# Optimization experiments

Measured on AMD Instinct MI355X. Metric: run time of the kernel, lower is better.

The kernel has to match this reference:

```python
import jax, jax.numpy as jnp
import numpy as np

T, B, IN = 64, 4096, 145
H1, H2 = 150, 32


def _lstm_layer(x, w_ih, w_hh, b_ih, b_hh):
    """Single LSTM layer, PyTorch gate order (i, f, g, o).
    x: (T, B, in_dim); w_ih: (4H, in_dim); w_hh: (4H, H); biases: (4H,).
    Returns hidden sequence (T, B, H)."""
    H = w_hh.shape[1]
    Bsz = x.shape[1]
    # Precompute input contribution for all timesteps at once (one big GEMM).
    xg = jnp.einsum('tbi,gi->tbg', x, w_ih) + (b_ih + b_hh)  # (T, B, 4H)
    w_hh_t = w_hh.T  # (H, 4H)

    def step(carry, xg_t):
        h, c = carry
        gates = xg_t + h @ w_hh_t  # (B, 4H)
        i, f, g, o = jnp.split(gates, 4, axis=-1)
        i = jax.nn.sigmoid(i)
        f = jax.nn.sigmoid(f)
        g = jnp.tanh(g)
        o = jax.nn.sigmoid(o)
        c = f * c + i * g
        h = o * jnp.tanh(c)
        return (h, c), h

    h0 = jnp.zeros((Bsz, H), x.dtype)
    c0 = jnp.zeros((Bsz, H), x.dtype)
    _, hs = jax.lax.scan(step, (h0, c0), xg)
    return hs  # (T, B, H)


def _init_lstm_params(key, in_dim, hidden):
    # PyTorch init: U(-k, k) with k = 1/sqrt(hidden)
    k = 1.0 / np.sqrt(hidden)
    ks = jax.random.split(key, 4)
    w_ih = jax.random.uniform(ks[0], (4 * hidden, in_dim), jnp.float32, -k, k)
    w_hh = jax.random.uniform(ks[1], (4 * hidden, hidden), jnp.float32, -k, k)
    b_ih = jax.random.uniform(ks[2], (4 * hidden,), jnp.float32, -k, k)
    b_hh = jax.random.uniform(ks[3], (4 * hidden,), jnp.float32, -k, k)
    return w_ih, w_hh, b_ih, b_hh


def setup_inputs() -> dict:
    key = jax.random.key(0)
    kx, k0, k1, k2 = jax.random.split(key, 4)
    x = jax.random.normal(kx, (T, B, IN), jnp.float32)
    w_ih_l0, w_hh_l0, b_ih_l0, b_hh_l0 = _init_lstm_params(k0, IN, H1)
    w_ih_l1, w_hh_l1, b_ih_l1, b_hh_l1 = _init_lstm_params(k1, H1, H1)
    w_ih_l2, w_hh_l2, b_ih_l2, b_hh_l2 = _init_lstm_params(k2, H1, H2)
    return {
        'x': x,
        'w_ih_l0': w_ih_l0, 'w_hh_l0': w_hh_l0, 'b_ih_l0': b_ih_l0, 'b_hh_l0': b_hh_l0,
        'w_ih_l1': w_ih_l1, 'w_hh_l1': w_hh_l1, 'b_ih_l1': b_ih_l1, 'b_hh_l1': b_hh_l1,
        'w_ih_l2': w_ih_l2, 'w_hh_l2': w_hh_l2, 'b_ih_l2': b_ih_l2, 'b_hh_l2': b_hh_l2,
    }


def reference(x,
              w_ih_l0, w_hh_l0, b_ih_l0, b_hh_l0,
              w_ih_l1, w_hh_l1, b_ih_l1, b_hh_l1,
              w_ih_l2, w_hh_l2, b_ih_l2, b_hh_l2):
    # temporal_model1: 2-layer LSTM (145 -> 150 -> 150)
    h = _lstm_layer(x, w_ih_l0, w_hh_l0, b_ih_l0, b_hh_l0)
    h = _lstm_layer(h, w_ih_l1, w_hh_l1, b_ih_l1, b_hh_l1)
    # temporal_model2: 1-layer LSTM (150 -> 32)
    out2 = _lstm_layer(h, w_ih_l2, w_hh_l2, b_ih_l2, b_hh_l2)
    return out2  # (T, B, 32)
```

## Files before the change

### kernel.cpp

```cpp
#include <hip/hip_runtime.h>


typedef _Float16 f16;
typedef _Float16 f16x8 __attribute__((ext_vector_type(8)));
typedef _Float16 f16x4 __attribute__((ext_vector_type(4)));
typedef float f32x4 __attribute__((ext_vector_type(4)));

#define T_STEPS 64
#define BATCH 4096

__device__ __forceinline__ float fexp(float x) {
  return __builtin_amdgcn_exp2f(x * 1.44269504088896340736f);
}
__device__ __forceinline__ float sigf(float x) {
  return __builtin_amdgcn_rcpf(1.0f + fexp(-x));
}
__device__ __forceinline__ float tanh_f(float x) {
  return 1.0f - 2.0f * __builtin_amdgcn_rcpf(1.0f + fexp(2.0f * x));
}

#define BAR_LGKM() asm volatile("s_waitcnt lgkmcnt(0)\n\ts_barrier" ::: "memory")

__global__ __launch_bounds__(256) void prep_w(
    const float* __restrict__ wih0, const float* __restrict__ bih0, const float* __restrict__ bhh0,
    const float* __restrict__ wih1, const float* __restrict__ bih1, const float* __restrict__ bhh1,
    f16* __restrict__ wprep0, f16* __restrict__ wprep1,
    float* __restrict__ bias0, float* __restrict__ bias1) {
  int idx = blockIdx.x * 256 + threadIdx.x;
  constexpr int WE = 640 * 168;
  if (idx < WE) {
    int c = idx / 168, k = idx - c * 168;
    int gate = c / 160, cg = c - gate * 160;
    float v = (cg < 150 && k < 145) ? wih0[(size_t)(gate * 150 + cg) * 145 + k] : 0.f;
    wprep0[idx] = (f16)v;
  } else if (idx < 2 * WE) {
    int e = idx - WE;
    int c = e / 168, k = e - c * 168;
    int gate = c / 160, cg = c - gate * 160;
    float v = (cg < 150 && k < 150) ? wih1[(size_t)(gate * 150 + cg) * 150 + k] : 0.f;
    wprep1[e] = (f16)v;
  } else if (idx < 2 * WE + 640) {
    int c = idx - 2 * WE;
    int gate = c / 160, cg = c - gate * 160;
    bias0[c] = (cg < 150) ? (bih0[gate * 150 + cg] + bhh0[gate * 150 + cg]) : 0.f;
  } else if (idx < 2 * WE + 1280) {
    int c = idx - 2 * WE - 640;
    int gate = c / 160, cg = c - gate * 160;
    bias1[c] = (cg < 150) ? (bih1[gate * 150 + cg] + bhh1[gate * 150 + cg]) : 0.f;
  }
}

template <int IN_DIM, int SRC_F16>
__global__ __launch_bounds__(512, 2) void gemm_xg3(
    const float* __restrict__ xin_f32, const f16* __restrict__ xin_f16,
    const f16* __restrict__ wprep, const float* __restrict__ bias_pre,
    f16* __restrict__ xg) {
  constexpr int ASTR = 168;
  __shared__ __align__(16) f16 A_lds[128 * ASTR];
  __shared__ __align__(16) float bias_lds[640];
  const int tid = threadIdx.x;
  const int mtile = blockIdx.x;
  const int g0 = mtile * 128;

  if constexpr (SRC_F16) {
#pragma unroll
    for (int q = 0; q < 6; ++q) {
      int i = q * 512 + tid;
      if (i < 2688)
        *(f16x8*)(&A_lds[i * 8]) = *(const f16x8*)(xin_f16 + (size_t)g0 * ASTR + (size_t)i * 8);
    }
  } else {
#pragma unroll
    for (int q = 0; q < 10; ++q) {
      int idx = q * 512 + tid;
      int r = idx / 40, c4 = (idx - r * 40) * 4;
      f16x4 o;
      if (c4 + 4 <= IN_DIM) {
        f32x4 v;
        __builtin_memcpy(&v, xin_f32 + (size_t)(g0 + r) * IN_DIM + c4, 16);
#pragma unroll
        for (int j = 0; j < 4; ++j) o[j] = (f16)v[j];
      } else {
#pragma unroll
        for (int j = 0; j < 4; ++j)
          o[j] = (c4 + j < IN_DIM) ? (f16)xin_f32[(size_t)(g0 + r) * IN_DIM + c4 + j] : (f16)0.f;
      }
      *(f16x4*)(&A_lds[r * ASTR + c4]) = o;
    }
  }
  if (tid < 160) *(f32x4*)(&bias_lds[tid * 4]) = *(const f32x4*)(bias_pre + tid * 4);
  __syncthreads();

  const int l = tid & 63, wv = tid >> 6;
  const int p = wv >> 1, cq = wv & 1;
  const int lrow = l & 15, lk8 = (l >> 4) * 8, r0 = (l >> 4) * 4;
  const int arow0 = (2 * p) * 16 + lrow;
  const size_t rg0 = (size_t)(mtile * 8 + 2 * p);

  const f16* wb = wprep + (size_t)(cq * 32 + lrow) * ASTR + lk8;

  f16x8 b0[5], b1[5], n0[5], n1[5];
#pragma unroll
  for (int kc = 0; kc < 5; ++kc) {
    b0[kc] = *(const f16x8*)(wb + kc * 32);
    b1[kc] = *(const f16x8*)(wb + 16 * ASTR + kc * 32);
  }

  for (int ch = 0; ch < 10; ++ch) {
    if (ch < 9) {
      const f16* wn = wb + (size_t)(ch + 1) * 64 * ASTR;
#pragma unroll
      for (int kc = 0; kc < 5; ++kc) {
        n0[kc] = *(const f16x8*)(wn + kc * 32);
        n1[kc] = *(const f16x8*)(wn + 16 * ASTR + kc * 32);
      }
    }
    const int c0 = ch * 64 + cq * 32 + lrow;
    const float bs0 = bias_lds[c0], bs1 = bias_lds[c0 + 16];
    f32x4 a00 = {bs0, bs0, bs0, bs0}, a01 = {bs1, bs1, bs1, bs1};
    f32x4 a10 = a00, a11 = a01;
#pragma unroll
    for (int kc = 0; kc < 5; ++kc) {
      f16x8 a0 = *(const f16x8*)(&A_lds[arow0 * ASTR + kc * 32 + lk8]);
      f16x8 a1 = *(const f16x8*)(&A_lds[(arow0 + 16) * ASTR + kc * 32 + lk8]);
      a00 = __builtin_amdgcn_mfma_f32_16x16x32_f16(a0, b0[kc], a00, 0, 0, 0);
      a01 = __builtin_amdgcn_mfma_f32_16x16x32_f16(a0, b1[kc], a01, 0, 0, 0);
      a10 = __builtin_amdgcn_mfma_f32_16x16x32_f16(a1, b0[kc], a10, 0, 0, 0);
      a11 = __builtin_amdgcn_mfma_f32_16x16x32_f16(a1, b1[kc], a11, 0, 0, 0);
    }
    {
      f16x4 o;
#pragma unroll
      for (int j = 0; j < 4; ++j) o[j] = (f16)a00[j];
      *(f16x4*)(xg + (rg0 * 640 + c0) * 16 + r0) = o;
#pragma unroll
      for (int j = 0; j < 4; ++j) o[j] = (f16)a01[j];
      *(f16x4*)(xg + (rg0 * 640 + c0 + 16) * 16 + r0) = o;
#pragma unroll
      for (int j = 0; j < 4; ++j) o[j] = (f16)a10[j];
      *(f16x4*)(xg + ((rg0 + 1) * 640 + c0) * 16 + r0) = o;
#pragma unroll
      for (int j = 0; j < 4; ++j) o[j] = (f16)a11[j];
      *(f16x4*)(xg + ((rg0 + 1) * 640 + c0 + 16) * 16 + r0) = o;
    }
#pragma unroll
    for (int kc = 0; kc < 5; ++kc) { b0[kc] = n0[kc]; b1[kc] = n1[kc]; }
  }
}

__global__ __launch_bounds__(640, 2) void lstm_rec(
    const f16* __restrict__ xg, const float* __restrict__ whh,
    f16* __restrict__ hout) {
  constexpr int H = 150, HSTR = 168, CPAD = 640;
  __shared__ __align__(16) f16 hbuf[2][16 * HSTR];
  const int tid = threadIdx.x;
  const int l = tid & 63, w = tid >> 6;
  const int lrow = l & 15, lk8 = (l >> 4) * 8, r0 = (l >> 4) * 4;
  const int col = w * 16 + lrow;
  const int bx = blockIdx.x, b0 = bx * 16;

  for (int i = tid; i < 2 * 16 * HSTR / 8; i += 640) {
    f16x8 z = {};
    *(f16x8*)(&hbuf[0][0] + (size_t)i * 8) = z;
  }

  f16x8 wh[4][5];
#pragma unroll
  for (int g = 0; g < 4; ++g)
#pragma unroll
    for (int kc = 0; kc < 5; ++kc) {
      f16x8 v;
#pragma unroll
      for (int j = 0; j < 8; ++j) {
        int k = kc * 32 + lk8 + j;
        float x = (col < H && k < H) ? whh[((size_t)g * H + col) * H + k] : 0.f;
        v[j] = (f16)x;
      }
      wh[g][kc] = v;
    }
  __syncthreads();

  float creg[4] = {0.f, 0.f, 0.f, 0.f};
  f16x4 pv[4];
#pragma unroll
  for (int g = 0; g < 4; ++g)
    pv[g] = *(const f16x4*)(xg + ((size_t)bx * CPAD + g * 160 + col) * 16 + r0);

  for (int t = 0; t < T_STEPS; ++t) {
    const int cur = t & 1, nxt = cur ^ 1;

    f32x4 acc[4];
#pragma unroll
    for (int g = 0; g < 4; ++g) {
#pragma unroll
      for (int j = 0; j < 4; ++j) acc[g][j] = (float)pv[g][j];
    }
    if (t + 1 < T_STEPS) {
#pragma unroll
      for (int g = 0; g < 4; ++g)
        pv[g] = *(const f16x4*)(xg + ((size_t)((t + 1) * 256 + bx) * CPAD + g * 160 + col) * 16 + r0);
    }
    if (t > 0 && tid < 336) {
      f16x8 v = *(const f16x8*)(&hbuf[cur][tid * 8]);
      *(f16x8*)(hout + ((size_t)(t - 1) * BATCH + b0) * 168 + (size_t)tid * 8) = v;
    }

#pragma unroll
    for (int kc = 0; kc < 5; ++kc) {
      f16x8 a = *(const f16x8*)(&hbuf[cur][lrow * HSTR + kc * 32 + lk8]);
#pragma unroll
      for (int g = 0; g < 4; ++g)
        acc[g] = __builtin_amdgcn_mfma_f32_16x16x32_f16(a, wh[g][kc], acc[g], 0, 0, 0);
    }

#pragma unroll
    for (int j = 0; j < 4; ++j) {
      float iv = sigf(acc[0][j]);
      float fv = sigf(acc[1][j]);
      float gv = tanh_f(acc[2][j]);
      float ov = sigf(acc[3][j]);
      float c = fv * creg[j] + iv * gv;
      creg[j] = c;
      float h = ov * tanh_f(c);
      hbuf[nxt][(r0 + j) * HSTR + col] = (f16)h;
    }

    BAR_LGKM();
  }
  if (tid < 336) {
    f16x8 v = *(const f16x8*)(&hbuf[0][tid * 8]);
    *(f16x8*)(hout + ((size_t)(T_STEPS - 1) * BATCH + b0) * 168 + (size_t)tid * 8) = v;
  }
}

template <int IN_DIM, int H, int MODE>
__global__ __launch_bounds__(512, 2) void lstm_layer(
    const float* __restrict__ xin_f32, const f16* __restrict__ xin_f16,
    const float* __restrict__ w_ih, const float* __restrict__ w_hh,
    const float* __restrict__ b_ih, const float* __restrict__ b_hh,
    f16* __restrict__ hout, float* __restrict__ yout) {
  constexpr int KX = (IN_DIM + 31) / 32;
  constexpr int XSTR = KX * 32 + 8;
  constexpr int KH = (H + 31) / 32;
  constexpr int HSTR = KH * 32 + 8;
  constexpr int NPAD = ((H + 31) / 32) * 32;
  constexpr int NT = NPAD / 32;
  constexpr int GROUPS = NPAD * 4;
  constexpr int UPD_ITERS = (GROUPS + 511) / 512;
  constexpr int XIN_ELEMS = 16 * IN_DIM;
  constexpr int QX = (XIN_ELEMS + 511) / 512;
  constexpr int STG = (16 * XSTR) / 8;
  constexpr int HCP = (16 * HSTR) / 8;
  static_assert(MODE == 0 || XSTR == 168, "");

  __shared__ __align__(16) f16 xbuf[2][16 * XSTR];
  __shared__ __align__(16) f16 hbuf[16 * HSTR];
  __shared__ __align__(16) float gates[NPAD * 84];

  const int tid = threadIdx.x;
  const int l = tid & 63;
  const int wv = tid >> 6;
  const int gate = wv >> 1;
  const int half = wv & 1;
  const int lrow = l & 15;
  const int lk8 = (l >> 4) * 8;
  const int r0 = (l >> 4) * 4;
  const int b0 = blockIdx.x * 16;

  {
    f16* xf = &xbuf[0][0];
    for (int i = tid; i < 2 * 16 * XSTR; i += 512) xf[i] = (f16)0.f;
    for (int i = tid; i < 16 * HSTR; i += 512) hbuf[i] = (f16)0.f;
  }
  const int rbase = half * (NPAD / 2) + lrow;
  float bias_reg[NT];
#pragma unroll
  for (int nt = 0; nt < NT; ++nt) {
    int n = rbase + nt * 16;
    bias_reg[nt] = (n < H) ? (b_ih[gate * H + n] + b_hh[gate * H + n]) : 0.f;
  }
  f16x8 wx[KX][NT], wh[KH][NT];
#pragma unroll
  for (int kc = 0; kc < KX; ++kc)
#pragma unroll
    for (int nt = 0; nt < NT; ++nt) {
      f16x8 wq;
#pragma unroll
      for (int j = 0; j < 8; ++j) {
        int k = kc * 32 + lk8 + j;
        int r = rbase + nt * 16;
        float v = (r < H && k < IN_DIM) ? w_ih[(size_t)(gate * H + r) * IN_DIM + k] : 0.f;
        wq[j] = (f16)v;
      }
      wx[kc][nt] = wq;
    }
#pragma unroll
  for (int kc = 0; kc < KH; ++kc)
#pragma unroll
    for (int nt = 0; nt < NT; ++nt) {
      f16x8 wq;
#pragma unroll
      for (int j = 0; j < 8; ++j) {
        int k = kc * 32 + lk8 + j;
        int r = rbase + nt * 16;
        float v = (r < H && k < H) ? w_hh[(size_t)(gate * H + r) * H + k] : 0.f;
        wq[j] = (f16)v;
      }
      wh[kc][nt] = wq;
    }

  if constexpr (MODE == 0) {
#pragma unroll
    for (int q = 0; q < QX; ++q) {
      int idx = q * 512 + tid;
      if (idx < XIN_ELEMS) {
        float v = xin_f32[(size_t)b0 * IN_DIM + idx];
        int r = idx / IN_DIM, c = idx - r * IN_DIM;
        xbuf[0][r * XSTR + c] = (f16)v;
      }
    }
  } else {
    if (tid < STG) {
      f16x8 v = *(const f16x8*)(xin_f16 + (size_t)b0 * 168 + tid * 8);
      *(f16x8*)(&xbuf[0][tid * 8]) = v;
    }
  }
  __syncthreads();

  float creg[UPD_ITERS][4];
#pragma unroll
  for (int it = 0; it < UPD_ITERS; ++it)
#pragma unroll
    for (int j = 0; j < 4; ++j) creg[it][j] = 0.f;

  float xv[QX];
  f16x8 pv;

  for (int t = 0; t < T_STEPS; ++t) {
    const int cur = t & 1, nxt = cur ^ 1;
    if (t + 1 < T_STEPS) {
      if constexpr (MODE == 0) {
        const float* src = xin_f32 + ((size_t)(t + 1) * BATCH + b0) * IN_DIM;
#pragma unroll
        for (int q = 0; q < QX; ++q) {
          int idx = q * 512 + tid;
          xv[q] = (idx < XIN_ELEMS) ? src[idx] : 0.f;
        }
      } else {
        if (tid < STG)
          pv = *(const f16x8*)(xin_f16 + ((size_t)(t + 1) * BATCH + b0) * 168 + tid * 8);
      }
    }
    if constexpr (MODE != 2) {
      if (t > 0 && tid < HCP) {
        f16x8 v = *(const f16x8*)(&hbuf[tid * 8]);
        *(f16x8*)(hout + ((size_t)(t - 1) * BATCH + b0) * 168 + tid * 8) = v;
      }
    }
    f32x4 acc[NT];
#pragma unroll
    for (int nt = 0; nt < NT; ++nt) {
      float b = bias_reg[nt];
      acc[nt] = f32x4{b, b, b, b};
    }
    {
      const f16* xb = &xbuf[cur][0];
#pragma unroll
      for (int kc = 0; kc < KX; ++kc) {
        f16x8 a = *(const f16x8*)(xb + lrow * XSTR + kc * 32 + lk8);
#pragma unroll
        for (int nt = 0; nt < NT; ++nt)
          acc[nt] = __builtin_amdgcn_mfma_f32_16x16x32_f16(a, wx[kc][nt], acc[nt], 0, 0, 0);
      }
#pragma unroll
      for (int kc = 0; kc < KH; ++kc) {
        f16x8 a = *(const f16x8*)(hbuf + lrow * HSTR + kc * 32 + lk8);
#pragma unroll
        for (int nt = 0; nt < NT; ++nt)
          acc[nt] = __builtin_amdgcn_mfma_f32_16x16x32_f16(a, wh[kc][nt], acc[nt], 0, 0, 0);
      }
    }
#pragma unroll
    for (int nt = 0; nt < NT; ++nt) {
      int n = half * (NPAD / 2) + nt * 16 + lrow;
      *(f32x4*)(&gates[n * 84 + gate * 20 + r0]) = acc[nt];
    }
    BAR_LGKM();
    if (t + 1 < T_STEPS) {
      if constexpr (MODE == 0) {
#pragma unroll
        for (int q = 0; q < QX; ++q) {
          int idx = q * 512 + tid;
          if (idx < XIN_ELEMS) {
            int r = idx / IN_DIM, c = idx - r * IN_DIM;
            xbuf[nxt][r * XSTR + c] = (f16)xv[q];
          }
        }
      } else {
        if (tid < STG) *(f16x8*)(&xbuf[nxt][tid * 8]) = pv;
      }
    }
#pragma unroll
    for (int it = 0; it < UPD_ITERS; ++it) {
      int grp = it * 512 + tid;
      if (grp < GROUPS) {
        int n = grp % NPAD;
        int rb = (grp / NPAD) * 4;
        if (n < H) {
          f32x4 gi = *(const f32x4*)(&gates[n * 84 + 0 + rb]);
          f32x4 gf = *(const f32x4*)(&gates[n * 84 + 20 + rb]);
          f32x4 gg = *(const f32x4*)(&gates[n * 84 + 40 + rb]);
          f32x4 go = *(const f32x4*)(&gates[n * 84 + 60 + rb]);
#pragma unroll
          for (int j = 0; j < 4; ++j) {
            float iv = sigf(gi[j]);
            float fv = sigf(gf[j]);
            float gv = tanh_f(gg[j]);
            float ov = sigf(go[j]);
            float c = fv * creg[it][j] + iv * gv;
            creg[it][j] = c;
            float h = ov * tanh_f(c);
            hbuf[(rb + j) * HSTR + n] = (f16)h;
            if constexpr (MODE == 2) {
              yout[((size_t)t * BATCH + b0 + rb + j) * 32 + n] = h;
            }
          }
        }
      }
    }
    BAR_LGKM();
  }
  if constexpr (MODE != 2) {
    if (tid < HCP) {
      f16x8 v = *(const f16x8*)(&hbuf[tid * 8]);
      *(f16x8*)(hout + ((size_t)(T_STEPS - 1) * BATCH + b0) * 168 + tid * 8) = v;
    }
  }
}

extern "C" void kernel_launch(void* const* d_in, const int* in_sizes, int n_in,
                              void* d_out, int out_size, void* d_ws, size_t ws_size,
                              hipStream_t stream) {
  const float* x = (const float*)d_in[0];
  const float* wih0 = (const float*)d_in[1];
  const float* whh0 = (const float*)d_in[2];
  const float* bih0 = (const float*)d_in[3];
  const float* bhh0 = (const float*)d_in[4];
  const float* wih1 = (const float*)d_in[5];
  const float* whh1 = (const float*)d_in[6];
  const float* bih1 = (const float*)d_in[7];
  const float* bhh1 = (const float*)d_in[8];
  const float* wih2 = (const float*)d_in[9];
  const float* whh2 = (const float*)d_in[10];
  const float* bih2 = (const float*)d_in[11];
  const float* bhh2 = (const float*)d_in[12];

  const size_t HSEQ_BYTES = (size_t)T_STEPS * BATCH * 168 * sizeof(f16);
  const size_t XG_BYTES = (size_t)T_STEPS * BATCH * 640 * sizeof(f16);
  const size_t WPREP_BYTES = (size_t)640 * 168 * sizeof(f16);
  const size_t NEED = HSEQ_BYTES + XG_BYTES + 2 * WPREP_BYTES + 2 * 640 * sizeof(float);
  f16* hws = (f16*)d_ws;
  float* out = (float*)d_out;

  if (ws_size >= NEED) {
    char* base = (char*)d_ws;
    f16* xgbuf = (f16*)(base + HSEQ_BYTES);
    f16* wprep0 = (f16*)(base + HSEQ_BYTES + XG_BYTES);
    f16* wprep1 = (f16*)(base + HSEQ_BYTES + XG_BYTES + WPREP_BYTES);
    float* bias0 = (float*)(base + HSEQ_BYTES + XG_BYTES + 2 * WPREP_BYTES);
    float* bias1 = bias0 + 640;

    prep_w<<<dim3(846), dim3(256), 0, stream>>>(wih0, bih0, bhh0, wih1, bih1, bhh1,
                                                wprep0, wprep1, bias0, bias1);
    dim3 gg(2048), gb(512);
    dim3 rg(BATCH / 16), rb(640);
    gemm_xg3<145, 0><<<gg, gb, 0, stream>>>(x, nullptr, wprep0, bias0, xgbuf);
    lstm_rec<<<rg, rb, 0, stream>>>(xgbuf, whh0, hws);
    gemm_xg3<150, 1><<<gg, gb, 0, stream>>>(nullptr, hws, wprep1, bias1, xgbuf);
    lstm_rec<<<rg, rb, 0, stream>>>(xgbuf, whh1, hws);
    lstm_layer<150, 32, 2><<<dim3(BATCH / 16), dim3(512), 0, stream>>>(
        nullptr, hws, wih2, whh2, bih2, bhh2, nullptr, out);
  } else {
    dim3 grid(BATCH / 16), block(512);
    lstm_layer<145, 150, 0><<<grid, block, 0, stream>>>(x, nullptr, wih0, whh0, bih0, bhh0, hws, nullptr);
    lstm_layer<150, 150, 1><<<grid, block, 0, stream>>>(nullptr, hws, wih1, whh1, bih1, bhh1, hws, nullptr);
    lstm_layer<150, 32, 2><<<grid, block, 0, stream>>>(nullptr, hws, wih2, whh2, bih2, bhh2, nullptr, out);
  }
}
```

Measured before the change: 748.9 us.

## Stage GEMM weight chunks through LDS and raise occupancy to four blocks

The input-projection GEMM kernel now loads each 64-column weight chunk cooperatively into shared memory and prefetches the next chunk into registers, instead of each wave keeping its own double-buffered weight fragments in registers. This frees registers, which lets the launch bound ask for four blocks per SM instead of two. The cost is extra LDS reads for the B operand, two barriers per chunk, and about 21KB more shared memory per block, which may limit how many blocks actually fit.

```diff
diff --git a/kernel.cpp b/kernel.cpp
--- a/kernel.cpp
+++ b/kernel.cpp
@@ -51,12 +51,13 @@
 }
 
 template <int IN_DIM, int SRC_F16>
-__global__ __launch_bounds__(512, 2) void gemm_xg3(
+__global__ __launch_bounds__(512, 4) void gemm_xg4(
     const float* __restrict__ xin_f32, const f16* __restrict__ xin_f16,
     const f16* __restrict__ wprep, const float* __restrict__ bias_pre,
     f16* __restrict__ xg) {
   constexpr int ASTR = 168;
   __shared__ __align__(16) f16 A_lds[128 * ASTR];
+  __shared__ __align__(16) f16 W_lds[64 * ASTR];
   __shared__ __align__(16) float bias_lds[640];
   const int tid = threadIdx.x;
   const int mtile = blockIdx.x;
@@ -89,33 +90,28 @@
     }
   }
   if (tid < 160) *(f32x4*)(&bias_lds[tid * 4]) = *(const f32x4*)(bias_pre + tid * 4);
-  __syncthreads();
+#pragma unroll
+  for (int q = 0; q < 3; ++q) {
+    int i = q * 512 + tid;
+    if (i < 1344) *(f16x8*)(&W_lds[i * 8]) = *(const f16x8*)(wprep + (size_t)i * 8);
+  }
+  BAR_LGKM();
 
   const int l = tid & 63, wv = tid >> 6;
   const int p = wv >> 1, cq = wv & 1;
   const int lrow = l & 15, lk8 = (l >> 4) * 8, r0 = (l >> 4) * 4;
   const int arow0 = (2 * p) * 16 + lrow;
-  const size_t rg0 = (size_t)(mtile * 8 + 2 * p);
-
-  const f16* wb = wprep + (size_t)(cq * 32 + lrow) * ASTR + lk8;
-
-  f16x8 b0[5], b1[5], n0[5], n1[5];
-#pragma unroll
-  for (int kc = 0; kc < 5; ++kc) {
-    b0[kc] = *(const f16x8*)(wb + kc * 32);
-    b1[kc] = *(const f16x8*)(wb + 16 * ASTR + kc * 32);
-  }
-
+  const int wrow0 = (2 * cq) * 16 + lrow;
+
+  f16x8 pv0, pv1, pv2;
   for (int ch = 0; ch < 10; ++ch) {
     if (ch < 9) {
-      const f16* wn = wb + (size_t)(ch + 1) * 64 * ASTR;
-#pragma unroll
-      for (int kc = 0; kc < 5; ++kc) {
-        n0[kc] = *(const f16x8*)(wn + kc * 32);
-        n1[kc] = *(const f16x8*)(wn + 16 * ASTR + kc * 32);
-      }
-    }
-    const int c0 = ch * 64 + cq * 32 + lrow;
+      const f16* wsrc = wprep + (size_t)(ch + 1) * 10752;
+      pv0 = *(const f16x8*)(wsrc + (size_t)tid * 8);
+      pv1 = *(const f16x8*)(wsrc + (size_t)(tid + 512) * 8);
+      if (tid < 320) pv2 = *(const f16x8*)(wsrc + (size_t)(tid + 1024) * 8);
+    }
+    const int c0 = ch * 64 + (2 * cq) * 16 + lrow;
     const float bs0 = bias_lds[c0], bs1 = bias_lds[c0 + 16];
     f32x4 a00 = {bs0, bs0, bs0, bs0}, a01 = {bs1, bs1, bs1, bs1};
     f32x4 a10 = a00, a11 = a01;
@@ -123,13 +119,16 @@
     for (int kc = 0; kc < 5; ++kc) {
       f16x8 a0 = *(const f16x8*)(&A_lds[arow0 * ASTR + kc * 32 + lk8]);
       f16x8 a1 = *(const f16x8*)(&A_lds[(arow0 + 16) * ASTR + kc * 32 + lk8]);
-      a00 = __builtin_amdgcn_mfma_f32_16x16x32_f16(a0, b0[kc], a00, 0, 0, 0);
-      a01 = __builtin_amdgcn_mfma_f32_16x16x32_f16(a0, b1[kc], a01, 0, 0, 0);
-      a10 = __builtin_amdgcn_mfma_f32_16x16x32_f16(a1, b0[kc], a10, 0, 0, 0);
-      a11 = __builtin_amdgcn_mfma_f32_16x16x32_f16(a1, b1[kc], a11, 0, 0, 0);
+      f16x8 b0 = *(const f16x8*)(&W_lds[wrow0 * ASTR + kc * 32 + lk8]);
+      f16x8 b1 = *(const f16x8*)(&W_lds[(wrow0 + 16) * ASTR + kc * 32 + lk8]);
+      a00 = __builtin_amdgcn_mfma_f32_16x16x32_f16(a0, b0, a00, 0, 0, 0);
+      a01 = __builtin_amdgcn_mfma_f32_16x16x32_f16(a0, b1, a01, 0, 0, 0);
+      a10 = __builtin_amdgcn_mfma_f32_16x16x32_f16(a1, b0, a10, 0, 0, 0);
+      a11 = __builtin_amdgcn_mfma_f32_16x16x32_f16(a1, b1, a11, 0, 0, 0);
     }
     {
       f16x4 o;
+      size_t rg0 = (size_t)(mtile * 8 + 2 * p);
 #pragma unroll
       for (int j = 0; j < 4; ++j) o[j] = (f16)a00[j];
       *(f16x4*)(xg + (rg0 * 640 + c0) * 16 + r0) = o;
@@ -143,8 +142,13 @@
       for (int j = 0; j < 4; ++j) o[j] = (f16)a11[j];
       *(f16x4*)(xg + ((rg0 + 1) * 640 + c0 + 16) * 16 + r0) = o;
     }
-#pragma unroll
-    for (int kc = 0; kc < 5; ++kc) { b0[kc] = n0[kc]; b1[kc] = n1[kc]; }
+    if (ch < 9) {
+      BAR_LGKM();
+      *(f16x8*)(&W_lds[tid * 8]) = pv0;
+      *(f16x8*)(&W_lds[(tid + 512) * 8]) = pv1;
+      if (tid < 320) *(f16x8*)(&W_lds[(tid + 1024) * 8]) = pv2;
+      BAR_LGKM();
+    }
   }
 }
 
@@ -474,9 +478,9 @@
                                                 wprep0, wprep1, bias0, bias1);
     dim3 gg(2048), gb(512);
     dim3 rg(BATCH / 16), rb(640);
-    gemm_xg3<145, 0><<<gg, gb, 0, stream>>>(x, nullptr, wprep0, bias0, xgbuf);
+    gemm_xg4<145, 0><<<gg, gb, 0, stream>>>(x, nullptr, wprep0, bias0, xgbuf);
     lstm_rec<<<rg, rb, 0, stream>>>(xgbuf, whh0, hws);
-    gemm_xg3<150, 1><<<gg, gb, 0, stream>>>(nullptr, hws, wprep1, bias1, xgbuf);
+    gemm_xg4<150, 1><<<gg, gb, 0, stream>>>(nullptr, hws, wprep1, bias1, xgbuf);
     lstm_rec<<<rg, rb, 0, stream>>>(xgbuf, whh1, hws);
     lstm_layer<150, 32, 2><<<dim3(BATCH / 16), dim3(512), 0, stream>>>(
         nullptr, hws, wih2, whh2, bih2, bhh2, nullptr, out);
```

Result: faster. 615.8 us (-17.8%).
